# Kernel optimization log

Hardware: AMD Instinct MI355X
Metric: run time of the kernel (lower is better)

Reference implementation:

```python
import jax, jax.numpy as jnp
import numpy as np

BS, N, FEAT = 4, 4096, 64
LN_EPS = 1e-5


def setup_inputs() -> dict:
    key = jax.random.key(0)
    k1, k2, k3 = jax.random.split(key, 3)
    positions = jax.random.normal(k1, (BS, N, 3), dtype=jnp.float32)
    # nn.Linear(n_point, feature_dim): weight (FEAT, N), bias (FEAT,)
    W = jax.random.normal(k2, (FEAT, N), dtype=jnp.float32) * (1.0 / np.sqrt(N))
    b = jax.random.normal(k3, (FEAT,), dtype=jnp.float32) * 0.02
    gamma = jnp.ones((FEAT,), dtype=jnp.float32)
    beta = jnp.zeros((FEAT,), dtype=jnp.float32)
    return {"positions": positions, "W": W, "b": b, "gamma": gamma, "beta": beta}


def reference(positions, W, b, gamma, beta):
    # all-pairs squared distances: (bs, N, N)
    diff = positions[:, :, None, :] - positions[:, None, :, :]  # (bs,N,N,3)
    sq = jnp.sum(diff * diff, axis=-1)                          # (bs,N,N)
    # safe sqrt (diagonal is exactly 0)
    safe = jnp.where(sq > 0, sq, 1.0)
    dist = jnp.where(sq > 0, jnp.sqrt(safe), 0.0)               # (bs,N,N)
    # Linear(N -> FEAT)
    x = jnp.einsum('bnm,fm->bnf', dist, W) + b                  # (bs,N,FEAT)
    # LayerNorm over last dim (biased variance, eps=1e-5)
    mu = jnp.mean(x, axis=-1, keepdims=True)
    var = jnp.mean((x - mu) ** 2, axis=-1, keepdims=True)
    xn = (x - mu) / jnp.sqrt(var + LN_EPS) * gamma + beta
    # SiLU
    return xn * jax.nn.sigmoid(xn)
```

## Files before the change

### kernel.cpp

```cpp
#include <hip/hip_runtime.h>


typedef float f32x4 __attribute__((ext_vector_type(4)));
typedef __bf16 bf16x8 __attribute__((ext_vector_type(8)));

union BF8 { bf16x8 v; uint4 u; };

#define N_PTS 4096
#define FEATD 64

__global__ void prep_kernel(const float* __restrict__ W,
                            const float* __restrict__ pos,
                            unsigned short* __restrict__ Wbt,
                            float* __restrict__ Pt) {
  int b = blockIdx.x, t = threadIdx.x;
  if (b < 128) {
    int gid = b * 256 + t;
    int f = gid >> 9, m8 = gid & 511;
    const float4* src = (const float4*)(W + (size_t)f * N_PTS + m8 * 8);
    float4 a = src[0], bb = src[1];
    BF8 o;
    o.v[0] = (__bf16)a.x;  o.v[1] = (__bf16)a.y;  o.v[2] = (__bf16)a.z;  o.v[3] = (__bf16)a.w;
    o.v[4] = (__bf16)bb.x; o.v[5] = (__bf16)bb.y; o.v[6] = (__bf16)bb.z; o.v[7] = (__bf16)bb.w;
    ((uint4*)Wbt)[(size_t)m8 * 64 + f] = o.u;
  } else {
    int bb = b - 128;
    int batch = bb >> 2, qtr = bb & 3;
    const float4* p4 = (const float4*)(pos + ((size_t)batch * N_PTS + qtr * 1024) * 3);
    float4 f0 = p4[t * 3 + 0], f1 = p4[t * 3 + 1], f2 = p4[t * 3 + 2];
    float4* Px = (float4*)(Pt + (size_t)(0 * 4 + batch) * N_PTS) + qtr * 256;
    float4* Py = (float4*)(Pt + (size_t)(1 * 4 + batch) * N_PTS) + qtr * 256;
    float4* Pz = (float4*)(Pt + (size_t)(2 * 4 + batch) * N_PTS) + qtr * 256;
    Px[t] = make_float4(f0.x, f0.w, f1.z, f2.y);
    Py[t] = make_float4(f0.y, f1.x, f1.w, f2.z);
    Pz[t] = make_float4(f0.z, f1.y, f2.x, f2.w);
  }
}

__device__ __forceinline__ void merge_and_epilogue(
    f32x4 (&acc)[2][4], f32x4* mbuf, int wave, int lane, int fx, int q,
    int batch, int rb, const float* bias, const float* gamma,
    const float* beta, float* out) {
  auto wr = [&](int rg) {
#pragma unroll
    for (int a = 0; a < 2; ++a)
#pragma unroll
      for (int t = 0; t < 4; ++t)
        mbuf[rg * 512 + (a * 4 + t) * 64 + lane] = acc[a][t];
  };
  auto rd = [&](int rg) {
#pragma unroll
    for (int a = 0; a < 2; ++a)
#pragma unroll
      for (int t = 0; t < 4; ++t)
        acc[a][t] += mbuf[rg * 512 + (a * 4 + t) * 64 + lane];
  };
  if (wave >= 4) wr(wave - 4);
  __syncthreads();
  if (wave < 4) rd(wave);
  __syncthreads();
  if (wave == 2 || wave == 3) wr(wave - 2);
  __syncthreads();
  if (wave < 2) rd(wave);
  __syncthreads();
  if (wave == 1) wr(0);
  __syncthreads();

  if (wave == 0) {
    rd(0);
    float bb[4], gg[4], be[4];
#pragma unroll
    for (int t = 0; t < 4; ++t) {
      bb[t] = bias[t * 16 + fx];
      gg[t] = gamma[t * 16 + fx];
      be[t] = beta[t * 16 + fx];
    }
    float* outB = out + ((size_t)batch * N_PTS + rb) * FEATD;
#pragma unroll
    for (int a = 0; a < 2; ++a) {
#pragma unroll
      for (int r = 0; r < 4; ++r) {
        float x[4], d[4];
#pragma unroll
        for (int t = 0; t < 4; ++t) x[t] = acc[a][t][r] + bb[t];
        float s = x[0] + x[1] + x[2] + x[3];
        s += __shfl_xor(s, 1); s += __shfl_xor(s, 2);
        s += __shfl_xor(s, 4); s += __shfl_xor(s, 8);
        float mu = s * (1.f / 64.f);
        float v = 0.f;
#pragma unroll
        for (int t = 0; t < 4; ++t) { d[t] = x[t] - mu; v += d[t] * d[t]; }
        v += __shfl_xor(v, 1); v += __shfl_xor(v, 2);
        v += __shfl_xor(v, 4); v += __shfl_xor(v, 8);
        float rstd = __builtin_amdgcn_rsqf(v * (1.f / 64.f) + 1e-5f);
        float* orow = outB + (a * 16 + q * 4 + r) * FEATD;
#pragma unroll
        for (int t = 0; t < 4; ++t) {
          float xn = d[t] * rstd * gg[t] + be[t];
          float y = xn * (1.f / (1.f + __expf(-xn)));
          orow[t * 16 + fx] = y;
        }
      }
    }
  }
}

__global__ __launch_bounds__(512, 4) void frp_kernel(
    const float* __restrict__ bias, const float* __restrict__ gamma,
    const float* __restrict__ beta, const unsigned short* __restrict__ Wbt,
    const float* __restrict__ Pt, float* __restrict__ out) {
  __shared__ f32x4 mbuf[4 * 512];

  const int tid = threadIdx.x;
  const int lane = tid & 63;
  const int wave = tid >> 6;
  const int fx = lane & 15;
  const int q = lane >> 4;

  const int batch = blockIdx.x >> 7;
  const int rb = (blockIdx.x & 127) * 32;

  const float* PxG = Pt + (size_t)(0 * 4 + batch) * N_PTS;
  const float* PyG = Pt + (size_t)(1 * 4 + batch) * N_PTS;
  const float* PzG = Pt + (size_t)(2 * 4 + batch) * N_PTS;
  const uint4* Wq = (const uint4*)Wbt;

  f32x4 acc[2][4];
#pragma unroll
  for (int a = 0; a < 2; ++a)
#pragma unroll
    for (int t = 0; t < 4; ++t) acc[a][t] = (f32x4){0.f, 0.f, 0.f, 0.f};

  const int G0 = wave * 4 + q;

  const int n0 = rb + fx;
  const float px0 = PxG[n0],      py0 = PyG[n0],      pz0 = PzG[n0];
  const float px1 = PxG[n0 + 16], py1 = PyG[n0 + 16], pz1 = PzG[n0 + 16];

#pragma unroll 2
  for (int c = 0; c < 16; ++c) {
    const int G = c * 32 + G0;
    const int m4 = G * 2;
    f32x4 xa = ((const f32x4*)PxG)[m4], xb = ((const f32x4*)PxG)[m4 + 1];
    f32x4 ya = ((const f32x4*)PyG)[m4], yb = ((const f32x4*)PyG)[m4 + 1];
    f32x4 za = ((const f32x4*)PzG)[m4], zb = ((const f32x4*)PzG)[m4 + 1];
    const uint4* wg = Wq + (size_t)G * 64 + fx;
    uint4 w0 = wg[0], w1 = wg[16], w2 = wg[32], w3 = wg[48];

    bf16x8 af0, af1;
    {
      f32x4 dx = xa - px0, dy = ya - py0, dz = za - pz0;
      f32x4 sq = dx * dx + dy * dy + dz * dz;
#pragma unroll
      for (int j = 0; j < 4; ++j) af0[j] = (__bf16)__builtin_amdgcn_sqrtf(sq[j]);
      dx = xb - px0; dy = yb - py0; dz = zb - pz0;
      sq = dx * dx + dy * dy + dz * dz;
#pragma unroll
      for (int j = 0; j < 4; ++j) af0[4 + j] = (__bf16)__builtin_amdgcn_sqrtf(sq[j]);
      dx = xa - px1; dy = ya - py1; dz = za - pz1;
      sq = dx * dx + dy * dy + dz * dz;
#pragma unroll
      for (int j = 0; j < 4; ++j) af1[j] = (__bf16)__builtin_amdgcn_sqrtf(sq[j]);
      dx = xb - px1; dy = yb - py1; dz = zb - pz1;
      sq = dx * dx + dy * dy + dz * dz;
#pragma unroll
      for (int j = 0; j < 4; ++j) af1[4 + j] = (__bf16)__builtin_amdgcn_sqrtf(sq[j]);
    }
    BF8 b0, b1, b2, b3;
    b0.u = w0; b1.u = w1; b2.u = w2; b3.u = w3;
    acc[0][0] = __builtin_amdgcn_mfma_f32_16x16x32_bf16(af0, b0.v, acc[0][0], 0, 0, 0);
    acc[1][0] = __builtin_amdgcn_mfma_f32_16x16x32_bf16(af1, b0.v, acc[1][0], 0, 0, 0);
    acc[0][1] = __builtin_amdgcn_mfma_f32_16x16x32_bf16(af0, b1.v, acc[0][1], 0, 0, 0);
    acc[1][1] = __builtin_amdgcn_mfma_f32_16x16x32_bf16(af1, b1.v, acc[1][1], 0, 0, 0);
    acc[0][2] = __builtin_amdgcn_mfma_f32_16x16x32_bf16(af0, b2.v, acc[0][2], 0, 0, 0);
    acc[1][2] = __builtin_amdgcn_mfma_f32_16x16x32_bf16(af1, b2.v, acc[1][2], 0, 0, 0);
    acc[0][3] = __builtin_amdgcn_mfma_f32_16x16x32_bf16(af0, b3.v, acc[0][3], 0, 0, 0);
    acc[1][3] = __builtin_amdgcn_mfma_f32_16x16x32_bf16(af1, b3.v, acc[1][3], 0, 0, 0);
  }

  merge_and_epilogue(acc, mbuf, wave, lane, fx, q, batch, rb,
                     bias, gamma, beta, out);
}

__global__ __launch_bounds__(512) void frp_fallback_kernel(
    const float* __restrict__ pos, const float* __restrict__ W,
    const float* __restrict__ bias, const float* __restrict__ gamma,
    const float* __restrict__ beta, float* __restrict__ out) {
  __shared__ f32x4 mbuf[4 * 512];
  const int tid = threadIdx.x;
  const int lane = tid & 63;
  const int wave = tid >> 6;
  const int fx = lane & 15;
  const int q = lane >> 4;
  const int batch = blockIdx.x >> 7;
  const int rb = (blockIdx.x & 127) * 32;
  const float* posB = pos + (size_t)batch * N_PTS * 3;

  f32x4 acc[2][4];
#pragma unroll
  for (int a = 0; a < 2; ++a)
#pragma unroll
    for (int t = 0; t < 4; ++t) acc[a][t] = (f32x4){0.f, 0.f, 0.f, 0.f};

  const int G0 = wave * 4 + q;
  const int n0 = rb + fx;
  const float px0 = posB[n0 * 3], py0 = posB[n0 * 3 + 1], pz0 = posB[n0 * 3 + 2];
  const float px1 = posB[(n0 + 16) * 3], py1 = posB[(n0 + 16) * 3 + 1],
              pz1 = posB[(n0 + 16) * 3 + 2];

  for (int c = 0; c < 16; ++c) {
    const int G = c * 32 + G0;
    bf16x8 af0, af1;
#pragma unroll
    for (int j = 0; j < 8; ++j) {
      const float* pk = posB + ((size_t)G * 8 + j) * 3;
      float kx = pk[0], ky = pk[1], kz = pk[2];
      float dx = kx - px0, dy = ky - py0, dz = kz - pz0;
      af0[j] = (__bf16)__builtin_amdgcn_sqrtf(dx * dx + dy * dy + dz * dz);
      dx = kx - px1; dy = ky - py1; dz = kz - pz1;
      af1[j] = (__bf16)__builtin_amdgcn_sqrtf(dx * dx + dy * dy + dz * dz);
    }
#pragma unroll
    for (int t = 0; t < 4; ++t) {
      const float* wr = W + (size_t)(t * 16 + fx) * N_PTS + G * 8;
      BF8 bw;
#pragma unroll
      for (int j = 0; j < 8; ++j) bw.v[j] = (__bf16)wr[j];
      acc[0][t] = __builtin_amdgcn_mfma_f32_16x16x32_bf16(af0, bw.v, acc[0][t], 0, 0, 0);
      acc[1][t] = __builtin_amdgcn_mfma_f32_16x16x32_bf16(af1, bw.v, acc[1][t], 0, 0, 0);
    }
  }
  merge_and_epilogue(acc, mbuf, wave, lane, fx, q, batch, rb,
                     bias, gamma, beta, out);
}

extern "C" void kernel_launch(void* const* d_in, const int* in_sizes, int n_in,
                              void* d_out, int out_size, void* d_ws, size_t ws_size,
                              hipStream_t stream) {
  const float* pos   = (const float*)d_in[0];
  const float* W     = (const float*)d_in[1];
  const float* bias  = (const float*)d_in[2];
  const float* gamma = (const float*)d_in[3];
  const float* beta  = (const float*)d_in[4];
  float* out = (float*)d_out;

  const size_t wb_bytes = (size_t)FEATD * N_PTS * sizeof(unsigned short);
  const size_t pt_bytes = (size_t)3 * 4 * N_PTS * sizeof(float);
  int use_ws = (d_ws != nullptr && ws_size >= wb_bytes + pt_bytes);

  if (use_ws) {
    unsigned short* Wbt = (unsigned short*)d_ws;
    float* Pt = (float*)((char*)d_ws + wb_bytes);
    prep_kernel<<<dim3(144), dim3(256), 0, stream>>>(W, pos, Wbt, Pt);
    frp_kernel<<<dim3(512), dim3(512), 0, stream>>>(bias, gamma, beta, Wbt, Pt, out);
  } else {
    frp_fallback_kernel<<<dim3(512), dim3(512), 0, stream>>>(pos, W, bias, gamma,
                                                             beta, out);
  }
}
```

Baseline: 92.77 us.

## Stage batch positions in LDS and software-prefetch W fragments

```diff
diff --git a/kernel.cpp b/kernel.cpp
--- a/kernel.cpp
+++ b/kernel.cpp
@@ -109,7 +109,7 @@
     const float* __restrict__ bias, const float* __restrict__ gamma,
     const float* __restrict__ beta, const unsigned short* __restrict__ Wbt,
     const float* __restrict__ Pt, float* __restrict__ out) {
-  __shared__ f32x4 mbuf[4 * 512];
+  __shared__ __align__(16) float Pl[3 * N_PTS];
 
   const int tid = threadIdx.x;
   const int lane = tid & 63;
@@ -120,10 +120,18 @@
   const int batch = blockIdx.x >> 7;
   const int rb = (blockIdx.x & 127) * 32;
 
-  const float* PxG = Pt + (size_t)(0 * 4 + batch) * N_PTS;
-  const float* PyG = Pt + (size_t)(1 * 4 + batch) * N_PTS;
-  const float* PzG = Pt + (size_t)(2 * 4 + batch) * N_PTS;
-  const uint4* Wq = (const uint4*)Wbt;
+#pragma unroll
+  for (int cc = 0; cc < 3; ++cc) {
+    const float4* s = (const float4*)(Pt + (size_t)(cc * 4 + batch) * N_PTS);
+    float4* d = (float4*)(Pl + cc * N_PTS);
+    d[tid] = s[tid];
+    d[tid + 512] = s[tid + 512];
+  }
+  __syncthreads();
+
+  const float* PxL = Pl;
+  const float* PyL = Pl + N_PTS;
+  const float* PzL = Pl + 2 * N_PTS;
 
   f32x4 acc[2][4];
 #pragma unroll
@@ -131,21 +139,27 @@
 #pragma unroll
     for (int t = 0; t < 4; ++t) acc[a][t] = (f32x4){0.f, 0.f, 0.f, 0.f};
 
+  const int n0 = rb + fx;
+  const float px0 = PxL[n0],      py0 = PyL[n0],      pz0 = PzL[n0];
+  const float px1 = PxL[n0 + 16], py1 = PyL[n0 + 16], pz1 = PzL[n0 + 16];
+
   const int G0 = wave * 4 + q;
-
-  const int n0 = rb + fx;
-  const float px0 = PxG[n0],      py0 = PyG[n0],      pz0 = PzG[n0];
-  const float px1 = PxG[n0 + 16], py1 = PyG[n0 + 16], pz1 = PzG[n0 + 16];
-
-#pragma unroll 2
+  const uint4* wgp = (const uint4*)Wbt + (size_t)G0 * 64 + fx;
+
+  uint4 w0n = wgp[0], w1n = wgp[16], w2n = wgp[32], w3n = wgp[48];
+
+#pragma unroll 1
   for (int c = 0; c < 16; ++c) {
-    const int G = c * 32 + G0;
-    const int m4 = G * 2;
-    f32x4 xa = ((const f32x4*)PxG)[m4], xb = ((const f32x4*)PxG)[m4 + 1];
-    f32x4 ya = ((const f32x4*)PyG)[m4], yb = ((const f32x4*)PyG)[m4 + 1];
-    f32x4 za = ((const f32x4*)PzG)[m4], zb = ((const f32x4*)PzG)[m4 + 1];
-    const uint4* wg = Wq + (size_t)G * 64 + fx;
-    uint4 w0 = wg[0], w1 = wg[16], w2 = wg[32], w3 = wg[48];
+    uint4 w0 = w0n, w1 = w1n, w2 = w2n, w3 = w3n;
+    if (c < 15) {
+      const uint4* wn = wgp + (size_t)(c + 1) * 2048;
+      w0n = wn[0]; w1n = wn[16]; w2n = wn[32]; w3n = wn[48];
+    }
+
+    const int m4 = (c * 32 + G0) * 2;
+    f32x4 xa = ((const f32x4*)PxL)[m4], xb = ((const f32x4*)PxL)[m4 + 1];
+    f32x4 ya = ((const f32x4*)PyL)[m4], yb = ((const f32x4*)PyL)[m4 + 1];
+    f32x4 za = ((const f32x4*)PzL)[m4], zb = ((const f32x4*)PzL)[m4 + 1];
 
     bf16x8 af0, af1;
     {
@@ -178,7 +192,8 @@
     acc[1][3] = __builtin_amdgcn_mfma_f32_16x16x32_bf16(af1, b3.v, acc[1][3], 0, 0, 0);
   }
 
-  merge_and_epilogue(acc, mbuf, wave, lane, fx, q, batch, rb,
+  __syncthreads();
+  merge_and_epilogue(acc, (f32x4*)Pl, wave, lane, fx, q, batch, rb,
                      bias, gamma, beta, out);
 }
 
```

After: 113.7 us. 1.23x slower.
